# Kernel optimization log

Measured on AMD Instinct MI355X. Metric: run time of the kernel, lower is better.

## Reference

```python
import math
import jax, jax.numpy as jnp
import numpy as np

N_SENSORS = 4760
K = 16
HID = 64
D_LAT = 1024
D_PROJ = 128
POS_DIM = 96
FACE_DIM = 32
OUT_CH = 1
N_HEADS = 4
HEAD_DIM = D_PROJ // N_HEADS
N_TOKENS = 6
NUM_BANDS = POS_DIM // 6
B = 16


def _sinusoidal_pos_encoding(positions, num_bands):
    # positions: (N,3) numpy -> (N, num_bands*2*3)
    freq = (2.0 ** np.arange(num_bands, dtype=np.float32))
    encs = []
    for d in range(3):
        scaled = positions[:, d:d + 1] * freq[None, :] * (math.pi / 100.0)
        encs.append(np.sin(scaled))
        encs.append(np.cos(scaled))
    return np.concatenate(encs, axis=-1).astype(np.float32)


def setup_inputs() -> dict:
    rng = np.random.default_rng(0)
    positions = rng.uniform(-100.0, 100.0, (N_SENSORS, 3)).astype(np.float32)
    # kNN graph by 3D euclidean distance
    d2 = ((positions[:, None, :] - positions[None, :, :]) ** 2).sum(-1)
    knn = np.argsort(d2, axis=1)[:, :K].astype(np.int32)
    face_ids = rng.integers(0, 6, N_SENSORS).astype(np.int32)
    pos_embed = _sinusoidal_pos_encoding(positions, NUM_BANDS)  # (N,96)

    key = jax.random.key(0)
    ks = jax.random.split(key, 20)
    def lin(k, din, dout):
        k1, k2 = jax.random.split(k)
        lim = 1.0 / math.sqrt(din)
        W = jax.random.uniform(k1, (din, dout), jnp.float32, -lim, lim)
        b = jax.random.uniform(k2, (dout,), jnp.float32, -lim, lim)
        return W, b

    W_nbr, b_nbr = lin(ks[0], 2 + POS_DIM + FACE_DIM, HID)
    W_ql, b_ql = lin(ks[1], POS_DIM + FACE_DIM, HID)
    W_lat, b_lat = lin(ks[2], D_LAT, D_PROJ)
    W_lf, b_lf = lin(ks[3], FACE_DIM, D_PROJ)
    W_qg, b_qg = lin(ks[4], POS_DIM + FACE_DIM, D_PROJ)
    W_k, b_k = lin(ks[5], D_PROJ, D_PROJ)
    W_v, b_v = lin(ks[6], D_PROJ, D_PROJ)
    W_go, b_go = lin(ks[7], D_PROJ, D_PROJ)
    W_m1, b_m1 = lin(ks[8], HID + D_PROJ, HID)
    W_m2, b_m2 = lin(ks[9], HID, OUT_CH)
    face_emb = jax.random.normal(ks[10], (6, FACE_DIM), jnp.float32)
    ln_g = jnp.ones((HID + D_PROJ,), jnp.float32)
    ln_b = jnp.zeros((HID + D_PROJ,), jnp.float32)

    x_flat = jax.random.normal(ks[11], (B, N_SENSORS, 2), jnp.float32)
    latent_seq = jax.random.normal(ks[12], (B, N_TOKENS, D_LAT), jnp.float32)
    mask = jax.random.randint(ks[13], (B, N_SENSORS), 0, 2, jnp.int32)

    return dict(x_flat=x_flat, latent_seq=latent_seq, pos_embed=jnp.asarray(pos_embed),
                face_emb=face_emb, W_nbr=W_nbr, b_nbr=b_nbr, W_ql=W_ql, b_ql=b_ql,
                W_lat=W_lat, b_lat=b_lat, W_lf=W_lf, b_lf=b_lf, W_qg=W_qg, b_qg=b_qg,
                W_k=W_k, b_k=b_k, W_v=W_v, b_v=b_v, W_go=W_go, b_go=b_go,
                ln_g=ln_g, ln_b=ln_b, W_m1=W_m1, b_m1=b_m1, W_m2=W_m2, b_m2=b_m2,
                mask=mask, knn_indices=jnp.asarray(knn), face_ids=jnp.asarray(face_ids))


def _forward(x_flat, latent_seq, pos_embed, face_emb,
             W_nbr, b_nbr, W_ql, b_ql, W_lat, b_lat, W_lf, b_lf,
             W_qg, b_qg, W_k, b_k, W_v, b_v, W_go, b_go,
             ln_g, ln_b, W_m1, b_m1, W_m2, b_m2,
             mask, knn_indices, face_ids):
    # Dense equivalent: compute prediction for every (b, n), zero out unmasked.
    # query: (N, pos+face)
    query = jnp.concatenate([pos_embed, face_emb[face_ids]], axis=-1)  # (N,128)

    # ---- local kNN attention ----
    nbr_values = x_flat[:, knn_indices, :]                 # (B,N,K,2)
    nbr_pos = pos_embed[knn_indices]                       # (N,K,96)
    nbr_face = face_emb[face_ids[knn_indices]]             # (N,K,32)
    nbr_static = jnp.broadcast_to(
        jnp.concatenate([nbr_pos, nbr_face], axis=-1)[None],
        (x_flat.shape[0], N_SENSORS, K, POS_DIM + FACE_DIM))
    nbr_feat = jnp.concatenate([nbr_values, nbr_static], axis=-1)  # (B,N,K,130)
    nbr_feat = nbr_feat @ W_nbr + b_nbr                    # (B,N,K,H)

    nbr_is_masked = mask[:, knn_indices] != 0              # (B,N,K) bool
    q_local = query @ W_ql + b_ql                          # (N,H)
    scale = HID ** (-0.5)
    logits = jnp.einsum('bnkh,nh->bnk', nbr_feat, q_local) * scale
    logits = jnp.where(nbr_is_masked, -10000.0, logits)
    attn = jax.nn.softmax(logits, axis=-1)
    local_feat = jnp.einsum('bnk,bnkh->bnh', attn, nbr_feat)  # (B,N,H)

    # ---- global cross-attention over 6 latent tokens ----
    latent_p = latent_seq @ W_lat + b_lat                  # (B,T,P)
    face_bias = face_emb[jnp.arange(N_TOKENS)] @ W_lf + b_lf  # (T,P)
    latent_kv = latent_p + face_bias[None]                 # (B,T,P)
    q_g = (query @ W_qg + b_qg).reshape(N_SENSORS, N_HEADS, HEAD_DIM)
    k_g = (latent_kv @ W_k + b_k).reshape(-1, N_TOKENS, N_HEADS, HEAD_DIM)
    v_g = (latent_kv @ W_v + b_v).reshape(-1, N_TOKENS, N_HEADS, HEAD_DIM)
    g_logits = jnp.einsum('nhd,bthd->bnht', q_g, k_g) * (HEAD_DIM ** (-0.5))
    g_attn = jax.nn.softmax(g_logits, axis=-1)
    g_feat = jnp.einsum('bnht,bthd->bnhd', g_attn, v_g)
    g_feat = g_feat.reshape(-1, N_SENSORS, D_PROJ) @ W_go + b_go  # (B,N,P)

    # ---- prediction MLP: LayerNorm -> Linear -> GELU -> Linear ----
    combined = jnp.concatenate([local_feat, g_feat], axis=-1)  # (B,N,H+P)
    mu = combined.mean(-1, keepdims=True)
    var = combined.var(-1, keepdims=True)
    normed = (combined - mu) * jax.lax.rsqrt(var + 1e-5) * ln_g + ln_b
    h = jax.nn.gelu(normed @ W_m1 + b_m1, approximate=False)
    preds = h @ W_m2 + b_m2                                # (B,N,out)

    return preds * (mask != 0)[..., None].astype(preds.dtype)


def reference(x_flat, latent_seq, pos_embed, face_emb,
              W_nbr, b_nbr, W_ql, b_ql, W_lat, b_lat, W_lf, b_lf,
              W_qg, b_qg, W_k, b_k, W_v, b_v, W_go, b_go,
              ln_g, ln_b, W_m1, b_m1, W_m2, b_m2,
              mask, knn_indices, face_ids):
    return _forward(x_flat, latent_seq, pos_embed, face_emb,
                    W_nbr, b_nbr, W_ql, b_ql, W_lat, b_lat, W_lf, b_lf,
                    W_qg, b_qg, W_k, b_k, W_v, b_v, W_go, b_go,
                    ln_g, ln_b, W_m1, b_m1, W_m2, b_m2,
                    mask, knn_indices, face_ids)
```

## Files before the change

### kernel.cpp

```cpp
#include <hip/hip_runtime.h>
#include <math.h>

#define NSN 4760
#define KNN 16
#define NT 6
#define NB 16
#define NGB 595

__device__ __forceinline__ float rl_f(float v, int lane) {
  return __builtin_bit_cast(float, __builtin_amdgcn_readlane(__builtin_bit_cast(int, v), lane));
}

__global__ void precompute_all(const float* __restrict__ pos_emb,
    const float* __restrict__ face_emb, const int* __restrict__ face_ids,
    const float* __restrict__ W_nbr, const float* __restrict__ b_nbr,
    const float* __restrict__ W_ql, const float* __restrict__ b_ql,
    const float* __restrict__ W_qg, const float* __restrict__ b_qg,
    const float* __restrict__ latent,
    const float* __restrict__ W_lat, const float* __restrict__ b_lat,
    const float* __restrict__ W_lf, const float* __restrict__ b_lf,
    const float* __restrict__ W_k, const float* __restrict__ b_k,
    const float* __restrict__ W_v, const float* __restrict__ b_v,
    const float* __restrict__ W_go, const float* __restrict__ b_go,
    const float* __restrict__ W_m1, const float* __restrict__ b_m1,
    const float* __restrict__ ln_g, const float* __restrict__ ln_b,
    float* __restrict__ S, float* __restrict__ qlocal,
    float* __restrict__ qg, float* __restrict__ c01, float2* __restrict__ SS,
    float* __restrict__ kg, float4* __restrict__ TBL, float* __restrict__ C)
{
  __shared__ __align__(16) float qT[8][128][4];
  __shared__ __align__(16) float lat[4][1024];
  __shared__ __align__(16) float kvS[4][128];
  __shared__ __align__(16) float vrow[4][128];
  __shared__ __align__(16) float vwl[4][4][128];
  const int bid = blockIdx.x;
  const int tid = threadIdx.x;

  if (bid < 149) {
    const int w = tid >> 6, lane = tid & 63;
    const int grp = bid * 8 + w;
    if (grp >= NSN / 4) return;
    const int n0 = grp * 4;
    #pragma unroll
    for (int si = 0; si < 4; ++si) {
      const int n = n0 + si;
      const int fid = face_ids[n];
      const int e1 = lane + 64;
      qT[w][lane][si] = pos_emb[n * 96 + lane];
      qT[w][e1][si] = (e1 < 96) ? pos_emb[n * 96 + e1] : face_emb[fid * 32 + (e1 - 96)];
    }
    const float bn = b_nbr[lane], bq = b_ql[lane];
    const float bg0 = b_qg[lane], bg1 = b_qg[lane + 64];
    float s[4], ql[4], g0[4], g1[4];
    #pragma unroll
    for (int si = 0; si < 4; ++si) { s[si] = bn; ql[si] = bq; g0[si] = bg0; g1[si] = bg1; }
    #pragma unroll 2
    for (int i = 0; i < 128; ++i) {
      const float wn  = W_nbr[(2 + i) * 64 + lane];
      const float wq  = W_ql[i * 64 + lane];
      const float wg0 = W_qg[i * 128 + lane];
      const float wg1 = W_qg[i * 128 + 64 + lane];
      const float4 qv = *(const float4*)&qT[w][i][0];
      s[0]  += qv.x * wn;  s[1]  += qv.y * wn;  s[2]  += qv.z * wn;  s[3]  += qv.w * wn;
      ql[0] += qv.x * wq;  ql[1] += qv.y * wq;  ql[2] += qv.z * wq;  ql[3] += qv.w * wq;
      g0[0] += qv.x * wg0; g0[1] += qv.y * wg0; g0[2] += qv.z * wg0; g0[3] += qv.w * wg0;
      g1[0] += qv.x * wg1; g1[1] += qv.y * wg1; g1[2] += qv.z * wg1; g1[3] += qv.w * wg1;
    }
    const float wn0 = W_nbr[lane], wn1 = W_nbr[64 + lane];
    #pragma unroll
    for (int si = 0; si < 4; ++si) {
      const int n = n0 + si;
      S[n * 64 + lane] = s[si];
      qlocal[n * 64 + lane] = ql[si];
      qg[n * 128 + lane] = g0[si];
      qg[n * 128 + 64 + lane] = g1[si];
      float p0 = wn0 * ql[si], p1 = wn1 * ql[si];
      #pragma unroll
      for (int o = 32; o; o >>= 1) { p0 += __shfl_xor(p0, o); p1 += __shfl_xor(p1, o); }
      if (lane == 0) { c01[2 * n] = p0; c01[2 * n + 1] = p1; }
    }
    const float gl = ln_g[lane];
    #pragma unroll
    for (int si = 0; si < 4; ++si) qT[w][lane][si] = s[si] * gl;
    float sm0 = 0.f, sm1 = 0.f, sm2 = 0.f, sm3 = 0.f;
    #pragma unroll 4
    for (int h = 0; h < 64; ++h) {
      const float w1v = W_m1[h * 64 + lane];
      const float4 sv = *(const float4*)&qT[w][h][0];
      sm0 += sv.x * w1v; sm1 += sv.y * w1v; sm2 += sv.z * w1v; sm3 += sv.w * w1v;
    }
    SS[(n0 + 0) * 64 + lane] = make_float2(s[0], sm0);
    SS[(n0 + 1) * 64 + lane] = make_float2(s[1], sm1);
    SS[(n0 + 2) * 64 + lane] = make_float2(s[2], sm2);
    SS[(n0 + 3) * 64 + lane] = make_float2(s[3], sm3);
  } else if (bid < 173) {
    const int team = tid >> 7, o = tid & 127;
    const int bt = (bid - 149) * 4 + team;
    const int t = bt % NT;
    for (int i = o; i < 1024; i += 128) lat[team][i] = latent[bt * 1024 + i];
    __syncthreads();
    float acc = b_lat[o] + b_lf[o];
    #pragma unroll 8
    for (int i = 0; i < 1024; ++i) acc += lat[team][i] * W_lat[i * 128 + o];
    #pragma unroll
    for (int i = 0; i < 32; ++i) acc += face_emb[t * 32 + i] * W_lf[i * 128 + o];
    kvS[team][o] = acc;
    __syncthreads();
    float kk = b_k[o], vv = b_v[o];
    #pragma unroll 4
    for (int i = 0; i < 128; ++i) {
      const float c = kvS[team][i];
      kk += c * W_k[i * 128 + o];
      vv += c * W_v[i * 128 + o];
    }
    kg[bt * 128 + o] = kk;
    vrow[team][o] = vv;
    __syncthreads();
    #pragma unroll
    for (int h = 0; h < 4; ++h) {
      float a = 0.f;
      #pragma unroll 8
      for (int i = 0; i < 32; ++i)
        a += vrow[team][h * 32 + i] * W_go[(h * 32 + i) * 128 + o];
      vwl[team][h][o] = a;
    }
    __syncthreads();
    if (o < 64) {
      #pragma unroll
      for (int h = 0; h < 4; ++h) {
        float m = 0.f;
        #pragma unroll 4
        for (int i = 0; i < 128; ++i)
          m += vwl[team][h][i] * ln_g[64 + i] * W_m1[(64 + i) * 64 + o];
        TBL[(bt * 4 + h) * 64 + o] =
            make_float4(vwl[team][h][2 * o], vwl[team][h][2 * o + 1], m, 0.f);
      }
    }
  } else {
    const int o = tid;
    if (o < 64) {
      float wa = 0.f, wb = 0.f;
      #pragma unroll 4
      for (int h = 0; h < 64; ++h) {
        const float gw = ln_g[h] * W_m1[h * 64 + o];
        wa += W_nbr[h] * gw;
        wb += W_nbr[64 + h] * gw;
      }
      C[o] = wa; C[64 + o] = wb;
      float g = 0.f, p = 0.f;
      #pragma unroll 4
      for (int d = 0; d < 192; ++d) {
        const float w1 = W_m1[d * 64 + o];
        g += ln_g[d] * w1;
        p += ln_b[d] * w1;
      }
      C[128 + o] = g; C[192 + o] = p + b_m1[o];
      float c1 = 0.f;
      #pragma unroll 4
      for (int i = 0; i < 128; ++i)
        c1 += b_go[i] * ln_g[64 + i] * W_m1[(64 + i) * 64 + o];
      C[256 + o] = c1;
    }
  }
}

__global__ void precompute_D(const int* __restrict__ knn,
    const float* __restrict__ S, const float* __restrict__ qlocal,
    float* __restrict__ D)
{
  const int idx = blockIdx.x * 256 + threadIdx.x;
  const int n = idx >> 4;
  if (n >= NSN) return;
  const int j = knn[idx];
  const float4* Sr = (const float4*)(S + j * 64);
  const float4* Qr = (const float4*)(qlocal + n * 64);
  float acc = 0.f;
  #pragma unroll 4
  for (int i = 0; i < 16; ++i) {
    const float4 a = Sr[i]; const float4 q = Qr[i];
    acc += a.x * q.x + a.y * q.y + a.z * q.z + a.w * q.w;
  }
  D[idx] = acc;
}

__launch_bounds__(256, 2)
__global__ void precompute_item(const int* __restrict__ knn,
    const float* __restrict__ D, const float* __restrict__ c01,
    const float* __restrict__ x_flat, const int* __restrict__ mask,
    const float* __restrict__ qg, const float* __restrict__ kg,
    float* __restrict__ ATT, float2* __restrict__ AX, float* __restrict__ GAW)
{
  const int i = blockIdx.x * 256 + threadIdx.x;
  if (i >= NB * NSN) return;
  const int b = i / NSN;
  const int n = i - b * NSN;

  int j[16];
  {
    const int4* kr = (const int4*)(knn + n * 16);
    const int4 a = kr[0], bb = kr[1], c = kr[2], d = kr[3];
    j[0]=a.x; j[1]=a.y; j[2]=a.z; j[3]=a.w;
    j[4]=bb.x; j[5]=bb.y; j[6]=bb.z; j[7]=bb.w;
    j[8]=c.x; j[9]=c.y; j[10]=c.z; j[11]=c.w;
    j[12]=d.x; j[13]=d.y; j[14]=d.z; j[15]=d.w;
  }
  float dg[16];
  {
    const float4* dr = (const float4*)(D + n * 16);
    const float4 a = dr[0], bb = dr[1], c = dr[2], d = dr[3];
    dg[0]=a.x; dg[1]=a.y; dg[2]=a.z; dg[3]=a.w;
    dg[4]=bb.x; dg[5]=bb.y; dg[6]=bb.z; dg[7]=bb.w;
    dg[8]=c.x; dg[9]=c.y; dg[10]=c.z; dg[11]=c.w;
    dg[12]=d.x; dg[13]=d.y; dg[14]=d.z; dg[15]=d.w;
  }
  const float2 cv = *(const float2*)(c01 + 2 * n);
  const float* xb = x_flat + (size_t)b * NSN * 2;
  const int* mb = mask + b * NSN;
  float x0[16], x1[16], lg[16];
  #pragma unroll 4
  for (int k = 0; k < 16; ++k) {
    const float2 xv = *(const float2*)(xb + 2 * j[k]);
    const int mk = mb[j[k]];
    x0[k] = xv.x; x1[k] = xv.y;
    const float l = (dg[k] + xv.x * cv.x + xv.y * cv.y) * 0.125f;
    lg[k] = (mk != 0) ? -10000.0f : l;
  }
  float mx = lg[0];
  #pragma unroll
  for (int k = 1; k < 16; ++k) mx = fmaxf(mx, lg[k]);
  float s = 0.f;
  #pragma unroll
  for (int k = 0; k < 16; ++k) { lg[k] = __expf(lg[k] - mx); s += lg[k]; }
  const float inv = 1.0f / s;
  float ax0 = 0.f, ax1 = 0.f;
  #pragma unroll
  for (int k = 0; k < 16; ++k) { lg[k] *= inv; ax0 += lg[k] * x0[k]; ax1 += lg[k] * x1[k]; }
  {
    float4* ao = (float4*)(ATT + (size_t)i * 16);
    ao[0] = make_float4(lg[0], lg[1], lg[2], lg[3]);
    ao[1] = make_float4(lg[4], lg[5], lg[6], lg[7]);
    ao[2] = make_float4(lg[8], lg[9], lg[10], lg[11]);
    ao[3] = make_float4(lg[12], lg[13], lg[14], lg[15]);
    AX[i] = make_float2(ax0, ax1);
  }

  const float* qgr = qg + n * 128;
  const float* kgb = kg + b * NT * 128;
  #pragma unroll 1
  for (int h = 0; h < 4; ++h) {
    float4 q[8];
    const float4* q4 = (const float4*)(qgr + h * 32);
    #pragma unroll
    for (int u = 0; u < 8; ++u) q[u] = q4[u];
    float p[NT];
    #pragma unroll
    for (int t = 0; t < NT; ++t) {
      const float4* k4 = (const float4*)(kgb + t * 128 + h * 32);
      float a = 0.f;
      #pragma unroll
      for (int u = 0; u < 8; ++u) {
        const float4 kv = k4[u];
        a += q[u].x * kv.x + q[u].y * kv.y + q[u].z * kv.z + q[u].w * kv.w;
      }
      p[t] = a * 0.17677669529663687f;
    }
    float m2 = p[0];
    #pragma unroll
    for (int t = 1; t < NT; ++t) m2 = fmaxf(m2, p[t]);
    float s2 = 0.f;
    #pragma unroll
    for (int t = 0; t < NT; ++t) { p[t] = __expf(p[t] - m2); s2 += p[t]; }
    const float i2 = 1.0f / s2;
    float* go = GAW + (size_t)i * 24 + h * 6;
    #pragma unroll
    for (int t = 0; t < NT; ++t) go[t] = p[t] * i2;
  }
}

__launch_bounds__(512, 2)
__global__ void fused_main(const int* __restrict__ mask,
    const int* __restrict__ knn, const float* __restrict__ Wnbr,
    const float2* __restrict__ SS, const float* __restrict__ ATT,
    const float2* __restrict__ AX, const float* __restrict__ GAW,
    const float4* __restrict__ TBL, const float* __restrict__ CONSTS,
    const float* __restrict__ bgo, const float* __restrict__ Wm2,
    const float* __restrict__ bm2, float* __restrict__ out)
{
  __shared__ __align__(16) float4 TBLl[NT * 4 * 64];

  const int tid = threadIdx.x;
  const int b = blockIdx.x / NGB;
  const int ng = blockIdx.x - b * NGB;
  {
    const float4* tb = TBL + b * (NT * 4 * 64);
    for (int i = tid; i < NT * 4 * 64; i += 512) TBLl[i] = tb[i];
  }
  __syncthreads();

  const int w = tid >> 6, lane = tid & 63;
  const int n = ng * 8 + w;
  const int item = b * NSN + n;

  const float wa  = CONSTS[lane],       wbc = CONSTS[64 + lane];
  const float cg  = CONSTS[128 + lane], cp  = CONSTS[192 + lane];
  const float cc1 = CONSTS[256 + lane];
  const float w0 = Wnbr[lane], w1 = Wnbr[64 + lane];
  const float2 bgov = *(const float2*)(bgo + 2 * lane);
  const float wm2 = Wm2[lane], bm2s = bm2[0];
  const int mself = mask[item];

  int jv = 0; float aw = 0.f;
  if (lane < 16) {
    jv = knn[n * 16 + lane];
    aw = ATT[(size_t)item * 16 + lane];
  }
  float gw = 0.f;
  if (lane < 24) gw = GAW[(size_t)item * 24 + lane];
  const float2 axv = AX[item];

  float lf = axv.x * w0 + axv.y * w1;
  float L  = axv.x * wa + axv.y * wbc;
  #pragma unroll
  for (int kb = 0; kb < 4; ++kb) {
    const int j0 = __builtin_amdgcn_readlane(jv, 4 * kb + 0);
    const int j1 = __builtin_amdgcn_readlane(jv, 4 * kb + 1);
    const int j2 = __builtin_amdgcn_readlane(jv, 4 * kb + 2);
    const int j3 = __builtin_amdgcn_readlane(jv, 4 * kb + 3);
    const float a0 = rl_f(aw, 4 * kb + 0);
    const float a1 = rl_f(aw, 4 * kb + 1);
    const float a2 = rl_f(aw, 4 * kb + 2);
    const float a3 = rl_f(aw, 4 * kb + 3);
    const float2 s0 = SS[j0 * 64 + lane];
    const float2 s1 = SS[j1 * 64 + lane];
    const float2 s2 = SS[j2 * 64 + lane];
    const float2 s3 = SS[j3 * 64 + lane];
    lf += a0 * s0.x + a1 * s1.x + a2 * s2.x + a3 * s3.x;
    L  += a0 * s0.y + a1 * s1.y + a2 * s2.y + a3 * s3.y;
  }

  float g0 = bgov.x, g1 = bgov.y, M = 0.f;
  #pragma unroll 2
  for (int t = 0; t < NT; ++t) {
    const float4 r0 = TBLl[(t * 4 + 0) * 64 + lane];
    const float4 r1 = TBLl[(t * 4 + 1) * 64 + lane];
    const float4 r2 = TBLl[(t * 4 + 2) * 64 + lane];
    const float4 r3 = TBLl[(t * 4 + 3) * 64 + lane];
    const float a0 = rl_f(gw, t);
    const float a1 = rl_f(gw, 6 + t);
    const float a2 = rl_f(gw, 12 + t);
    const float a3 = rl_f(gw, 18 + t);
    g0 += a0 * r0.x + a1 * r1.x + a2 * r2.x + a3 * r3.x;
    g1 += a0 * r0.y + a1 * r1.y + a2 * r2.y + a3 * r3.y;
    M  += a0 * r0.z + a1 * r1.z + a2 * r2.z + a3 * r3.z;
  }

  float s1 = lf + g0 + g1;
  float s2 = lf * lf + g0 * g0 + g1 * g1;
  #pragma unroll
  for (int o = 32; o; o >>= 1) { s1 += __shfl_xor(s1, o); s2 += __shfl_xor(s2, o); }
  const float mu  = s1 * (1.0f / 192.0f);
  const float var = s2 * (1.0f / 192.0f) - mu * mu;
  const float rinv = rsqrtf(var + 1e-5f);

  const float m1 = rinv * (L + M + cc1 - mu * cg) + cp;
  const float gelu = 0.5f * m1 * (1.0f + erff(m1 * 0.7071067811865476f));
  float pr = gelu * wm2;
  #pragma unroll
  for (int o = 32; o; o >>= 1) pr += __shfl_xor(pr, o);
  float res = pr + bm2s;
  if (mself == 0) res = 0.f;
  if (lane == 0) out[item] = res;
}

extern "C" void kernel_launch(void* const* d_in, const int* in_sizes, int n_in,
                              void* d_out, int out_size, void* d_ws, size_t ws_size,
                              hipStream_t stream) {
  (void)in_sizes; (void)n_in; (void)out_size; (void)ws_size;
  const float* x_flat   = (const float*)d_in[0];
  const float* latent   = (const float*)d_in[1];
  const float* pos_emb  = (const float*)d_in[2];
  const float* face_emb = (const float*)d_in[3];
  const float* W_nbr = (const float*)d_in[4];
  const float* b_nbr = (const float*)d_in[5];
  const float* W_ql  = (const float*)d_in[6];
  const float* b_ql  = (const float*)d_in[7];
  const float* W_lat = (const float*)d_in[8];
  const float* b_lat = (const float*)d_in[9];
  const float* W_lf  = (const float*)d_in[10];
  const float* b_lf  = (const float*)d_in[11];
  const float* W_qg  = (const float*)d_in[12];
  const float* b_qg  = (const float*)d_in[13];
  const float* W_k   = (const float*)d_in[14];
  const float* b_k   = (const float*)d_in[15];
  const float* W_v   = (const float*)d_in[16];
  const float* b_v   = (const float*)d_in[17];
  const float* W_go  = (const float*)d_in[18];
  const float* b_go  = (const float*)d_in[19];
  const float* ln_g  = (const float*)d_in[20];
  const float* ln_b  = (const float*)d_in[21];
  const float* W_m1  = (const float*)d_in[22];
  const float* b_m1  = (const float*)d_in[23];
  const float* W_m2  = (const float*)d_in[24];
  const float* b_m2  = (const float*)d_in[25];
  const int* mask     = (const int*)d_in[26];
  const int* knn      = (const int*)d_in[27];
  const int* face_ids = (const int*)d_in[28];
  float* out = (float*)d_out;

  float* ws = (float*)d_ws;
  float* S      = ws;  ws += NSN * 64;
  float* qlocal = ws;  ws += NSN * 64;
  float* qgb    = ws;  ws += NSN * 128;
  float* c01    = ws;  ws += NSN * 2;
  float2* SSt   = (float2*)ws;  ws += NSN * 64 * 2;
  float* kgb    = ws;  ws += NB * NT * 128;
  float4* TBLt  = (float4*)ws;  ws += NB * NT * 4 * 64 * 4;
  float* CONSTS = ws;  ws += 5 * 64;
  float* Dt     = ws;  ws += NSN * KNN;
  float* ATTt   = ws;  ws += NB * NSN * KNN;
  float2* AXt   = (float2*)ws;  ws += NB * NSN * 2;
  float* GAWt   = ws;  ws += NB * NSN * 24;

  precompute_all<<<174, 512, 0, stream>>>(pos_emb, face_emb, face_ids,
      W_nbr, b_nbr, W_ql, b_ql, W_qg, b_qg,
      latent, W_lat, b_lat, W_lf, b_lf, W_k, b_k, W_v, b_v,
      W_go, b_go, W_m1, b_m1, ln_g, ln_b,
      S, qlocal, qgb, c01, SSt, kgb, TBLt, CONSTS);
  precompute_D<<<(NSN * KNN + 255) / 256, 256, 0, stream>>>(knn, S, qlocal, Dt);
  precompute_item<<<(NB * NSN + 255) / 256, 256, 0, stream>>>(knn, Dt, c01,
      x_flat, mask, qgb, kgb, ATTt, AXt, GAWt);
  fused_main<<<NB * NGB, 512, 0, stream>>>(mask, knn, W_nbr,
      SSt, ATTt, AXt, GAWt, TBLt, CONSTS, b_go, W_m2, b_m2, out);
}
```

Baseline: 297.1 us.

## Spread precompute work across more blocks and raise fused_main occupancy bound

```diff
diff --git a/kernel.cpp b/kernel.cpp
--- a/kernel.cpp
+++ b/kernel.cpp
@@ -28,113 +28,104 @@
     float* __restrict__ qg, float* __restrict__ c01, float2* __restrict__ SS,
     float* __restrict__ kg, float4* __restrict__ TBL, float* __restrict__ C)
 {
-  __shared__ __align__(16) float qT[8][128][4];
-  __shared__ __align__(16) float lat[4][1024];
-  __shared__ __align__(16) float kvS[4][128];
-  __shared__ __align__(16) float vrow[4][128];
-  __shared__ __align__(16) float vwl[4][4][128];
+  __shared__ __align__(16) float qL[8][128];
+  __shared__ __align__(16) float lat[1024];
+  __shared__ __align__(16) float part[4][128];
+  __shared__ __align__(16) float kvS[128];
+  __shared__ __align__(16) float vrow[128];
+  __shared__ __align__(16) float vwl[4][128];
+  __shared__ __align__(16) float ghl[128];
   const int bid = blockIdx.x;
   const int tid = threadIdx.x;
 
-  if (bid < 149) {
+  if (bid < 595) {
     const int w = tid >> 6, lane = tid & 63;
-    const int grp = bid * 8 + w;
-    if (grp >= NSN / 4) return;
-    const int n0 = grp * 4;
-    #pragma unroll
-    for (int si = 0; si < 4; ++si) {
-      const int n = n0 + si;
-      const int fid = face_ids[n];
-      const int e1 = lane + 64;
-      qT[w][lane][si] = pos_emb[n * 96 + lane];
-      qT[w][e1][si] = (e1 < 96) ? pos_emb[n * 96 + e1] : face_emb[fid * 32 + (e1 - 96)];
-    }
-    const float bn = b_nbr[lane], bq = b_ql[lane];
-    const float bg0 = b_qg[lane], bg1 = b_qg[lane + 64];
-    float s[4], ql[4], g0[4], g1[4];
-    #pragma unroll
-    for (int si = 0; si < 4; ++si) { s[si] = bn; ql[si] = bq; g0[si] = bg0; g1[si] = bg1; }
+    const int n = bid * 8 + w;
+    const int fid = face_ids[n];
+    const int e1 = lane + 64;
+    qL[w][lane] = pos_emb[n * 96 + lane];
+    qL[w][e1] = (e1 < 96) ? pos_emb[n * 96 + e1] : face_emb[fid * 32 + (e1 - 96)];
+    float s  = b_nbr[lane], ql = b_ql[lane];
+    float g0 = b_qg[lane],  g1 = b_qg[lane + 64];
     #pragma unroll 2
     for (int i = 0; i < 128; ++i) {
-      const float wn  = W_nbr[(2 + i) * 64 + lane];
-      const float wq  = W_ql[i * 64 + lane];
-      const float wg0 = W_qg[i * 128 + lane];
-      const float wg1 = W_qg[i * 128 + 64 + lane];
-      const float4 qv = *(const float4*)&qT[w][i][0];
-      s[0]  += qv.x * wn;  s[1]  += qv.y * wn;  s[2]  += qv.z * wn;  s[3]  += qv.w * wn;
-      ql[0] += qv.x * wq;  ql[1] += qv.y * wq;  ql[2] += qv.z * wq;  ql[3] += qv.w * wq;
-      g0[0] += qv.x * wg0; g0[1] += qv.y * wg0; g0[2] += qv.z * wg0; g0[3] += qv.w * wg0;
-      g1[0] += qv.x * wg1; g1[1] += qv.y * wg1; g1[2] += qv.z * wg1; g1[3] += qv.w * wg1;
-    }
-    const float wn0 = W_nbr[lane], wn1 = W_nbr[64 + lane];
-    #pragma unroll
-    for (int si = 0; si < 4; ++si) {
-      const int n = n0 + si;
-      S[n * 64 + lane] = s[si];
-      qlocal[n * 64 + lane] = ql[si];
-      qg[n * 128 + lane] = g0[si];
-      qg[n * 128 + 64 + lane] = g1[si];
-      float p0 = wn0 * ql[si], p1 = wn1 * ql[si];
+      const float qi = qL[w][i];
+      s  += qi * W_nbr[(2 + i) * 64 + lane];
+      ql += qi * W_ql[i * 64 + lane];
+      g0 += qi * W_qg[i * 128 + lane];
+      g1 += qi * W_qg[i * 128 + 64 + lane];
+    }
+    S[n * 64 + lane] = s;
+    qlocal[n * 64 + lane] = ql;
+    qg[n * 128 + lane] = g0;
+    qg[n * 128 + 64 + lane] = g1;
+    float p0 = W_nbr[lane] * ql, p1 = W_nbr[64 + lane] * ql;
+    #pragma unroll
+    for (int o = 32; o; o >>= 1) { p0 += __shfl_xor(p0, o); p1 += __shfl_xor(p1, o); }
+    if (lane == 0) { c01[2 * n] = p0; c01[2 * n + 1] = p1; }
+    qL[w][lane] = s * ln_g[lane];
+    float sm = 0.f;
+    #pragma unroll 2
+    for (int h = 0; h < 64; ++h) {
+      sm += qL[w][h] * W_m1[h * 64 + lane];
+    }
+    SS[n * 64 + lane] = make_float2(s, sm);
+  } else if (bid < 691) {
+    const int bt = bid - 595;
+    const int t = bt % NT;
+    const int chunk = tid >> 7, o = tid & 127;
+    for (int i = tid; i < 1024; i += 512) lat[i] = latent[bt * 1024 + i];
+    if (tid < 128) ghl[tid] = ln_g[64 + tid];
+    __syncthreads();
+    {
+      float acc = 0.f;
+      const int i0 = chunk * 256;
+      #pragma unroll 4
+      for (int i = 0; i < 256; ++i)
+        acc += lat[i0 + i] * W_lat[(i0 + i) * 128 + o];
+      part[chunk][o] = acc;
+    }
+    __syncthreads();
+    if (tid < 128) {
+      float acc = part[0][o] + part[1][o] + part[2][o] + part[3][o]
+                + b_lat[o] + b_lf[o];
       #pragma unroll
-      for (int o = 32; o; o >>= 1) { p0 += __shfl_xor(p0, o); p1 += __shfl_xor(p1, o); }
-      if (lane == 0) { c01[2 * n] = p0; c01[2 * n + 1] = p1; }
-    }
-    const float gl = ln_g[lane];
-    #pragma unroll
-    for (int si = 0; si < 4; ++si) qT[w][lane][si] = s[si] * gl;
-    float sm0 = 0.f, sm1 = 0.f, sm2 = 0.f, sm3 = 0.f;
-    #pragma unroll 4
-    for (int h = 0; h < 64; ++h) {
-      const float w1v = W_m1[h * 64 + lane];
-      const float4 sv = *(const float4*)&qT[w][h][0];
-      sm0 += sv.x * w1v; sm1 += sv.y * w1v; sm2 += sv.z * w1v; sm3 += sv.w * w1v;
-    }
-    SS[(n0 + 0) * 64 + lane] = make_float2(s[0], sm0);
-    SS[(n0 + 1) * 64 + lane] = make_float2(s[1], sm1);
-    SS[(n0 + 2) * 64 + lane] = make_float2(s[2], sm2);
-    SS[(n0 + 3) * 64 + lane] = make_float2(s[3], sm3);
-  } else if (bid < 173) {
-    const int team = tid >> 7, o = tid & 127;
-    const int bt = (bid - 149) * 4 + team;
-    const int t = bt % NT;
-    for (int i = o; i < 1024; i += 128) lat[team][i] = latent[bt * 1024 + i];
-    __syncthreads();
-    float acc = b_lat[o] + b_lf[o];
-    #pragma unroll 8
-    for (int i = 0; i < 1024; ++i) acc += lat[team][i] * W_lat[i * 128 + o];
-    #pragma unroll
-    for (int i = 0; i < 32; ++i) acc += face_emb[t * 32 + i] * W_lf[i * 128 + o];
-    kvS[team][o] = acc;
-    __syncthreads();
-    float kk = b_k[o], vv = b_v[o];
-    #pragma unroll 4
-    for (int i = 0; i < 128; ++i) {
-      const float c = kvS[team][i];
-      kk += c * W_k[i * 128 + o];
-      vv += c * W_v[i * 128 + o];
-    }
-    kg[bt * 128 + o] = kk;
-    vrow[team][o] = vv;
-    __syncthreads();
-    #pragma unroll
-    for (int h = 0; h < 4; ++h) {
+      for (int i = 0; i < 32; ++i) acc += face_emb[t * 32 + i] * W_lf[i * 128 + o];
+      kvS[o] = acc;
+    }
+    __syncthreads();
+    {
+      const float* Wx = (chunk < 2) ? W_k : W_v;
+      const int i0 = (chunk & 1) * 64;
+      float acc = 0.f;
+      #pragma unroll 4
+      for (int i = 0; i < 64; ++i)
+        acc += kvS[i0 + i] * Wx[(i0 + i) * 128 + o];
+      part[chunk][o] = acc;
+    }
+    __syncthreads();
+    if (tid < 128) {
+      kg[bt * 128 + o] = part[0][o] + part[1][o] + b_k[o];
+    } else if (tid < 256) {
+      vrow[o] = part[2][o] + part[3][o] + b_v[o];
+    }
+    __syncthreads();
+    {
       float a = 0.f;
       #pragma unroll 8
       for (int i = 0; i < 32; ++i)
-        a += vrow[team][h * 32 + i] * W_go[(h * 32 + i) * 128 + o];
-      vwl[team][h][o] = a;
-    }
-    __syncthreads();
-    if (o < 64) {
-      #pragma unroll
-      for (int h = 0; h < 4; ++h) {
-        float m = 0.f;
-        #pragma unroll 4
-        for (int i = 0; i < 128; ++i)
-          m += vwl[team][h][i] * ln_g[64 + i] * W_m1[(64 + i) * 64 + o];
-        TBL[(bt * 4 + h) * 64 + o] =
-            make_float4(vwl[team][h][2 * o], vwl[team][h][2 * o + 1], m, 0.f);
-      }
+        a += vrow[chunk * 32 + i] * W_go[(chunk * 32 + i) * 128 + o];
+      vwl[chunk][o] = a;
+    }
+    __syncthreads();
+    if (tid < 256) {
+      const int h = tid >> 6, oo = tid & 63;
+      float m = 0.f;
+      #pragma unroll 4
+      for (int i = 0; i < 128; ++i)
+        m += vwl[h][i] * ghl[i] * W_m1[(64 + i) * 64 + oo];
+      TBL[(bt * 4 + h) * 64 + oo] =
+          make_float4(vwl[h][2 * oo], vwl[h][2 * oo + 1], m, 0.f);
     }
   } else {
     const int o = tid;
@@ -277,7 +268,7 @@
   }
 }
 
-__launch_bounds__(512, 2)
+__launch_bounds__(512, 4)
 __global__ void fused_main(const int* __restrict__ mask,
     const int* __restrict__ knn, const float* __restrict__ Wnbr,
     const float2* __restrict__ SS, const float* __restrict__ ATT,
@@ -421,7 +412,7 @@
   float2* AXt   = (float2*)ws;  ws += NB * NSN * 2;
   float* GAWt   = ws;  ws += NB * NSN * 24;
 
-  precompute_all<<<174, 512, 0, stream>>>(pos_emb, face_emb, face_ids,
+  precompute_all<<<692, 512, 0, stream>>>(pos_emb, face_emb, face_ids,
       W_nbr, b_nbr, W_ql, b_ql, W_qg, b_qg,
       latent, W_lat, b_lat, W_lf, b_lf, W_k, b_k, W_v, b_v,
       W_go, b_go, W_m1, b_m1, ln_g, ln_b,
```

Result: faster. 269.9 us (-9.2%).
